# Optimization experiments

Hardware: AMD Instinct MI355X
Metric: run time of the kernel (lower is better)

Reference implementation:

```python
import jax, jax.numpy as jnp
import numpy as np

D_MODEL = 1024
NHEAD = 16
HEAD_DIM = D_MODEL // NHEAD


def setup_inputs() -> dict:
    key = jax.random.key(0)
    ks = jax.random.split(key, 11)
    B, S = 2, 2048
    s = 1.0 / np.sqrt(D_MODEL)
    return {
        "query": jax.random.normal(ks[0], (B, S, D_MODEL), jnp.float32),
        "key": jax.random.normal(ks[1], (B, S, D_MODEL), jnp.float32),
        "value": jax.random.normal(ks[2], (B, S, D_MODEL), jnp.float32),
        "wq_w": jax.random.normal(ks[3], (D_MODEL, D_MODEL), jnp.float32) * s,
        "wq_b": jax.random.normal(ks[4], (D_MODEL,), jnp.float32) * s,
        "wk_w": jax.random.normal(ks[5], (D_MODEL, D_MODEL), jnp.float32) * s,
        "wk_b": jax.random.normal(ks[6], (D_MODEL,), jnp.float32) * s,
        "wv_w": jax.random.normal(ks[7], (D_MODEL, D_MODEL), jnp.float32) * s,
        "wv_b": jax.random.normal(ks[8], (D_MODEL,), jnp.float32) * s,
        "wo_w": jax.random.normal(ks[9], (D_MODEL, D_MODEL), jnp.float32) * s,
        "wo_b": jax.random.normal(ks[10], (D_MODEL,), jnp.float32) * s,
    }


def reference(query, key, value, wq_w, wq_b, wk_w, wk_b, wv_w, wv_b, wo_w, wo_b):
    B, S, _ = query.shape
    # torch Linear: x @ W.T + b
    def proj(x, w, b):
        y = x @ w.T + b
        return y.reshape(B, S, NHEAD, HEAD_DIM).transpose(0, 2, 1, 3)  # [B,H,S,Dh]

    Q = proj(query, wq_w, wq_b)
    K = proj(key, wk_w, wk_b)
    V = proj(value, wv_w, wv_b)

    scale = 1.0 / np.sqrt(HEAD_DIM).astype(np.float32)
    scores = jnp.einsum("bhqd,bhkd->bhqk", Q, K) * scale  # [B,H,S,S]
    causal = jnp.tril(jnp.ones((S, S), dtype=bool))
    scores = jnp.where(causal, scores, -jnp.inf)
    attn = jax.nn.softmax(scores, axis=-1)
    out = jnp.einsum("bhqk,bhkd->bhqd", attn, V)  # [B,H,S,Dh]
    out = out.transpose(0, 2, 1, 3).reshape(B, S, D_MODEL)
    return out @ wo_w.T + wo_b
```

## Files before the change

kernel.cpp:

```cpp
#include <hip/hip_runtime.h>
#include <stdint.h>

#define D_MODEL 1024
#define S_LEN   2048
#define NHEAD   16
#define HEAD_DIM 64
#define BATCH   2
#define M_TOT   (BATCH * S_LEN)
#define Q_SCALE 0.18033688011112042f

using bf16x8 = __attribute__((ext_vector_type(8))) short;
using f32x4  = __attribute__((ext_vector_type(4))) float;

__device__ __forceinline__ unsigned short f2bf(float f) {
  union { float f; unsigned int u; } v; v.f = f;
  unsigned int u = v.u;
  return (unsigned short)((u + 0x7FFFu + ((u >> 16) & 1u)) >> 16);
}
__device__ __forceinline__ unsigned int pkbf(float a, float b) {
#if __has_builtin(__builtin_amdgcn_cvt_pk_bf16_f32)
  auto p = __builtin_amdgcn_cvt_pk_bf16_f32(a, b);
  union { decltype(p) v; unsigned int u; } c; c.v = p;
  return c.u;
#else
  return (unsigned int)f2bf(a) | ((unsigned int)f2bf(b) << 16);
#endif
}
__device__ __forceinline__ bf16x8 cvt8(const float* p) {
  const float4 a = *(const float4*)p;
  const float4 b = *(const float4*)(p + 4);
  union { unsigned int u[4]; bf16x8 v; } r;
  r.u[0] = pkbf(a.x, a.y); r.u[1] = pkbf(a.z, a.w);
  r.u[2] = pkbf(b.x, b.y); r.u[3] = pkbf(b.z, b.w);
  return r.v;
}
__device__ __forceinline__ float fexp2(float x) {
#if __has_builtin(__builtin_amdgcn_exp2f)
  return __builtin_amdgcn_exp2f(x);
#else
  return __expf(x * 0.69314718055994531f);
#endif
}
__device__ __forceinline__ void async16(const unsigned short* g, short* l) {
  __builtin_amdgcn_global_load_lds(
      reinterpret_cast<const __attribute__((address_space(1))) unsigned int*>(
          reinterpret_cast<uintptr_t>(g)),
      reinterpret_cast<__attribute__((address_space(3))) unsigned int*>(
          reinterpret_cast<uintptr_t>(l)),
      16, 0, 0);
}

__device__ __forceinline__ void swap32(unsigned int& x, unsigned int& y) {
#if __has_builtin(__builtin_amdgcn_permlane32_swap)
  auto r = __builtin_amdgcn_permlane32_swap(x, y, false, false);
  x = (unsigned int)r[0]; y = (unsigned int)r[1];
#else
  const int lane = threadIdx.x & 63;
  unsigned int sx = (unsigned int)__shfl_xor((int)x, 32);
  unsigned int sy = (unsigned int)__shfl_xor((int)y, 32);
  unsigned int nx = (lane & 32) ? sy : x;
  unsigned int ny = (lane & 32) ? y : sx;
  x = nx; y = ny;
#endif
}
__device__ __forceinline__ void swap16(unsigned int& x, unsigned int& y) {
#if __has_builtin(__builtin_amdgcn_permlane16_swap)
  auto r = __builtin_amdgcn_permlane16_swap(x, y, false, false);
  x = (unsigned int)r[0]; y = (unsigned int)r[1];
#else
  const int lane = threadIdx.x & 63;
  unsigned int sx = (unsigned int)__shfl_xor((int)x, 16);
  unsigned int sy = (unsigned int)__shfl_xor((int)y, 16);
  unsigned int nx = (lane & 16) ? sy : x;
  unsigned int ny = (lane & 16) ? y : sx;
  x = nx; y = ny;
#endif
}

#define LDK 40

__global__ __launch_bounds__(256)
void cast_all(const float* __restrict__ wq, const float* __restrict__ wk,
              const float* __restrict__ wv, const float* __restrict__ wo,
              const float* __restrict__ q, const float* __restrict__ k,
              const float* __restrict__ v,
              unsigned short* __restrict__ wb,
              unsigned short* __restrict__ qb, unsigned short* __restrict__ kb,
              unsigned short* __restrict__ vb)
{
  const int z = blockIdx.y;
  const float* src;
  unsigned short* d;
  size_t n;
  switch (z) {
    case 0: src = wq; d = wb;                                   n = (size_t)D_MODEL * D_MODEL; break;
    case 1: src = wk; d = wb + (size_t)1 * D_MODEL * D_MODEL;   n = (size_t)D_MODEL * D_MODEL; break;
    case 2: src = wv; d = wb + (size_t)2 * D_MODEL * D_MODEL;   n = (size_t)D_MODEL * D_MODEL; break;
    case 3: src = wo; d = wb + (size_t)3 * D_MODEL * D_MODEL;   n = (size_t)D_MODEL * D_MODEL; break;
    case 4: src = q;  d = qb;                                   n = (size_t)M_TOT * D_MODEL;   break;
    case 5: src = k;  d = kb;                                   n = (size_t)M_TOT * D_MODEL;   break;
    default: src = v; d = vb;                                   n = (size_t)M_TOT * D_MODEL;   break;
  }
  const size_t i = ((size_t)blockIdx.x * 256 + threadIdx.x) * 8;
  if (i < n) *(bf16x8*)(d + i) = cvt8(src + i);
}

__device__ __forceinline__ void gemm_tile_lds(const unsigned short* __restrict__ A,
                                              const unsigned short* __restrict__ W,
                                              int m0, int n0,
                                              short* As, short* Bs,
                                              f32x4 acc[4][4])
{
  const int t    = threadIdx.x;
  const int lane = t & 63;
  const int w    = t >> 6;
  const int quad = lane >> 4;
  const int l16  = lane & 15;
  const int wm   = (w >> 1) * 64;
  const int wn   = (w & 1) * 64;
  const int srow = w * 16 + (lane >> 2);
  const int scol = (lane & 3) * 8;

  for (int mt = 0; mt < 4; ++mt)
    for (int nt = 0; nt < 4; ++nt)
      acc[mt][nt] = f32x4{0.f, 0.f, 0.f, 0.f};

  for (int kt = 0; kt < D_MODEL / 32; ++kt) {
    const int kc = kt * 32 + scol;
    __syncthreads();
    async16(A + (size_t)(m0 + srow)      * D_MODEL + kc, As + srow * 32 + scol);
    async16(A + (size_t)(m0 + 64 + srow) * D_MODEL + kc, As + (64 + srow) * 32 + scol);
    async16(W + (size_t)(n0 + srow)      * D_MODEL + kc, Bs + srow * 32 + scol);
    async16(W + (size_t)(n0 + 64 + srow) * D_MODEL + kc, Bs + (64 + srow) * 32 + scol);
    __syncthreads();

    bf16x8 af[4], bfr[4];
    for (int mt = 0; mt < 4; ++mt)
      af[mt] = *(const bf16x8*)(As + (wm + mt * 16 + l16) * 32 + quad * 8);
    for (int nt = 0; nt < 4; ++nt)
      bfr[nt] = *(const bf16x8*)(Bs + (wn + nt * 16 + l16) * 32 + quad * 8);
    for (int mt = 0; mt < 4; ++mt)
      for (int nt = 0; nt < 4; ++nt)
        acc[mt][nt] = __builtin_amdgcn_mfma_f32_16x16x32_bf16(af[mt], bfr[nt], acc[mt][nt], 0, 0, 0);
  }
}

__device__ __forceinline__ void gemm_tile_f32(const float* __restrict__ A,
                                              const unsigned short* __restrict__ W,
                                              int m0, int n0,
                                              short* As, short* Bs,
                                              f32x4 acc[4][4])
{
  const int t    = threadIdx.x;
  const int lane = t & 63;
  const int w    = t >> 6;
  const int quad = lane >> 4;
  const int l16  = lane & 15;
  const int wm   = (w >> 1) * 64;
  const int wn   = (w & 1) * 64;
  const int srow = t >> 2;
  const int scol = (t & 3) * 8;

  for (int mt = 0; mt < 4; ++mt)
    for (int nt = 0; nt < 4; ++nt)
      acc[mt][nt] = f32x4{0.f, 0.f, 0.f, 0.f};

  for (int kt = 0; kt < D_MODEL / 32; ++kt) {
    const int kc = kt * 32 + scol;
    const bf16x8 a0 = cvt8(A + (size_t)(m0 + srow)      * D_MODEL + kc);
    const bf16x8 a1 = cvt8(A + (size_t)(m0 + srow + 64) * D_MODEL + kc);
    const bf16x8 b0 = *(const bf16x8*)(W + (size_t)(n0 + srow)      * D_MODEL + kc);
    const bf16x8 b1 = *(const bf16x8*)(W + (size_t)(n0 + srow + 64) * D_MODEL + kc);
    __syncthreads();
    *(bf16x8*)(As + (srow)      * LDK + scol) = a0;
    *(bf16x8*)(As + (srow + 64) * LDK + scol) = a1;
    *(bf16x8*)(Bs + (srow)      * LDK + scol) = b0;
    *(bf16x8*)(Bs + (srow + 64) * LDK + scol) = b1;
    __syncthreads();

    bf16x8 af[4], bfr[4];
    for (int mt = 0; mt < 4; ++mt)
      af[mt] = *(const bf16x8*)(As + (wm + mt * 16 + l16) * LDK + quad * 8);
    for (int nt = 0; nt < 4; ++nt)
      bfr[nt] = *(const bf16x8*)(Bs + (wn + nt * 16 + l16) * LDK + quad * 8);
    for (int mt = 0; mt < 4; ++mt)
      for (int nt = 0; nt < 4; ++nt)
        acc[mt][nt] = __builtin_amdgcn_mfma_f32_16x16x32_bf16(af[mt], bfr[nt], acc[mt][nt], 0, 0, 0);
  }
}

__device__ __forceinline__ void qkv_epilogue(int z, int m0, int n0,
                                             const float* __restrict__ bias,
                                             float scale,
                                             unsigned short* __restrict__ dst,
                                             f32x4 acc[4][4])
{
  const int t    = threadIdx.x;
  const int lane = t & 63;
  const int w    = t >> 6;
  const int quad = lane >> 4;
  const int l16  = lane & 15;
  const int wm   = (w >> 1) * 64;
  const int wn   = (w & 1) * 64;

  for (int nt = 0; nt < 4; ++nt) {
    const int n = n0 + wn + nt * 16 + l16;
    const float bb = bias[n];
    const int h = n >> 6, d = n & 63;
    for (int mt = 0; mt < 4; ++mt) {
      for (int r = 0; r < 4; ++r) {
        const int m = m0 + wm + mt * 16 + quad * 4 + r;
        const int b = m >> 11, s = m & 2047;
        const unsigned short val = f2bf((acc[mt][nt][r] + bb) * scale);
        if (z < 2)
          dst[((size_t)((b * NHEAD + h) * S_LEN + s)) * HEAD_DIM + d] = val;
        else
          dst[((size_t)((b * NHEAD + h) * HEAD_DIM + d)) * S_LEN + s] = val;
      }
    }
  }
}

__global__ __launch_bounds__(256)
void qkv_fast(const unsigned short* __restrict__ qb,
              const unsigned short* __restrict__ kb,
              const unsigned short* __restrict__ vb,
              const unsigned short* __restrict__ wqb,
              const unsigned short* __restrict__ wkb,
              const unsigned short* __restrict__ wvb,
              const float* __restrict__ bq, const float* __restrict__ bk,
              const float* __restrict__ bv,
              unsigned short* __restrict__ Qh, unsigned short* __restrict__ Kh,
              unsigned short* __restrict__ VhT)
{
  __shared__ __attribute__((aligned(16))) short As[128 * 32];
  __shared__ __attribute__((aligned(16))) short Bs[128 * 32];
  const int z = blockIdx.z;
  const unsigned short* A    = (z == 0) ? qb  : (z == 1) ? kb  : vb;
  const unsigned short* W    = (z == 0) ? wqb : (z == 1) ? wkb : wvb;
  const float*          bias = (z == 0) ? bq  : (z == 1) ? bk  : bv;
  unsigned short*       dst  = (z == 0) ? Qh  : (z == 1) ? Kh  : VhT;
  const float           scale = (z == 0) ? Q_SCALE : 1.0f;

  const int m0 = blockIdx.x * 128, n0 = blockIdx.y * 128;
  f32x4 acc[4][4];
  gemm_tile_lds(A, W, m0, n0, As, Bs, acc);
  qkv_epilogue(z, m0, n0, bias, scale, dst, acc);
}

__global__ __launch_bounds__(256)
void qkv_slow(const float* __restrict__ query, const float* __restrict__ key,
              const float* __restrict__ value,
              const unsigned short* __restrict__ wqb,
              const unsigned short* __restrict__ wkb,
              const unsigned short* __restrict__ wvb,
              const float* __restrict__ bq, const float* __restrict__ bk,
              const float* __restrict__ bv,
              unsigned short* __restrict__ Qh, unsigned short* __restrict__ Kh,
              unsigned short* __restrict__ VhT)
{
  __shared__ __attribute__((aligned(16))) short As[128 * LDK];
  __shared__ __attribute__((aligned(16))) short Bs[128 * LDK];
  const int z = blockIdx.z;
  const float*          A    = (z == 0) ? query : (z == 1) ? key : value;
  const unsigned short* W    = (z == 0) ? wqb   : (z == 1) ? wkb : wvb;
  const float*          bias = (z == 0) ? bq    : (z == 1) ? bk  : bv;
  unsigned short*       dst  = (z == 0) ? Qh    : (z == 1) ? Kh  : VhT;
  const float           scale = (z == 0) ? Q_SCALE : 1.0f;

  const int m0 = blockIdx.x * 128, n0 = blockIdx.y * 128;
  f32x4 acc[4][4];
  gemm_tile_f32(A, W, m0, n0, As, Bs, acc);
  qkv_epilogue(z, m0, n0, bias, scale, dst, acc);
}

__global__ __launch_bounds__(256)
void out_proj(const unsigned short* __restrict__ Oh,
              const unsigned short* __restrict__ wob,
              const float* __restrict__ bo,
              float* __restrict__ dst)
{
  __shared__ __attribute__((aligned(16))) short As[64 * 32];
  __shared__ __attribute__((aligned(16))) short Bs[128 * 32];
  const int m0 = blockIdx.x * 64, n0 = blockIdx.y * 128;

  const int t    = threadIdx.x;
  const int lane = t & 63;
  const int w    = t >> 6;
  const int quad = lane >> 4;
  const int l16  = lane & 15;
  const int wm   = (w >> 1) * 32;
  const int wn   = (w & 1) * 64;
  const int srow = t >> 2;
  const int scol = (t & 3) * 8;

  f32x4 acc[2][4];
  for (int mt = 0; mt < 2; ++mt)
    for (int nt = 0; nt < 4; ++nt)
      acc[mt][nt] = f32x4{0.f, 0.f, 0.f, 0.f};

  for (int kt = 0; kt < D_MODEL / 32; ++kt) {
    const int kc = kt * 32 + scol;
    __syncthreads();
    async16(Oh  + (size_t)(m0 + srow)      * D_MODEL + kc, As + srow * 32 + scol);
    async16(wob + (size_t)(n0 + srow)      * D_MODEL + kc, Bs + srow * 32 + scol);
    async16(wob + (size_t)(n0 + 64 + srow) * D_MODEL + kc, Bs + (64 + srow) * 32 + scol);
    __syncthreads();

    bf16x8 af[2], bfr[4];
    for (int mt = 0; mt < 2; ++mt)
      af[mt] = *(const bf16x8*)(As + (wm + mt * 16 + l16) * 32 + quad * 8);
    for (int nt = 0; nt < 4; ++nt)
      bfr[nt] = *(const bf16x8*)(Bs + (wn + nt * 16 + l16) * 32 + quad * 8);
    for (int mt = 0; mt < 2; ++mt)
      for (int nt = 0; nt < 4; ++nt)
        acc[mt][nt] = __builtin_amdgcn_mfma_f32_16x16x32_bf16(af[mt], bfr[nt], acc[mt][nt], 0, 0, 0);
  }

  for (int nt = 0; nt < 4; ++nt) {
    const int n = n0 + wn + nt * 16 + l16;
    const float bb = bo[n];
    for (int mt = 0; mt < 2; ++mt)
      for (int r = 0; r < 4; ++r) {
        const int m = m0 + wm + mt * 16 + quad * 4 + r;
        dst[(size_t)m * D_MODEL + n] = acc[mt][nt][r] + bb;
      }
  }
}

struct Frags { bf16x8 ka0, ka1, kb0, kb1, v0, v1, v2, v3; };
struct StageRegs { bf16x8 k0, k1, k2, k3, v0, v1, v2, v3; };

#define KS_LD 72
#define VT_LD 136

__device__ __forceinline__ StageRegs load_stage(const unsigned short* __restrict__ Kb,
                                                const unsigned short* __restrict__ Vb,
                                                int k0, int kr, int kc, int vd, int vc) {
  StageRegs r;
  r.k0 = *(const bf16x8*)(Kb + (size_t)(k0 + kr)      * HEAD_DIM + kc);
  r.k1 = *(const bf16x8*)(Kb + (size_t)(k0 + kr + 32) * HEAD_DIM + kc);
  r.k2 = *(const bf16x8*)(Kb + (size_t)(k0 + kr + 64) * HEAD_DIM + kc);
  r.k3 = *(const bf16x8*)(Kb + (size_t)(k0 + kr + 96) * HEAD_DIM + kc);
  r.v0 = *(const bf16x8*)(Vb + (size_t)(vd)      * S_LEN + k0 + vc);
  r.v1 = *(const bf16x8*)(Vb + (size_t)(vd + 16) * S_LEN + k0 + vc);
  r.v2 = *(const bf16x8*)(Vb + (size_t)(vd + 32) * S_LEN + k0 + vc);
  r.v3 = *(const bf16x8*)(Vb + (size_t)(vd + 48) * S_LEN + k0 + vc);
  return r;
}
__device__ __forceinline__ void write_stage(const StageRegs& r, short* Ks, short* Vts,
                                            int kr, int kc, int vd, int vc) {
  *(bf16x8*)(Ks + (kr)      * KS_LD + kc) = r.k0;
  *(bf16x8*)(Ks + (kr + 32) * KS_LD + kc) = r.k1;
  *(bf16x8*)(Ks + (kr + 64) * KS_LD + kc) = r.k2;
  *(bf16x8*)(Ks + (kr + 96) * KS_LD + kc) = r.k3;
  *(bf16x8*)(Vts + (vd)      * VT_LD + vc) = r.v0;
  *(bf16x8*)(Vts + (vd + 16) * VT_LD + vc) = r.v1;
  *(bf16x8*)(Vts + (vd + 32) * VT_LD + vc) = r.v2;
  *(bf16x8*)(Vts + (vd + 48) * VT_LD + vc) = r.v3;
}
__device__ __forceinline__ Frags lds_frags(const short* Ks, const short* Vts,
                                           int c, int quad, int l16) {
  Frags f;
  const short* kp = Ks + (c * 32 + l16) * KS_LD + quad * 8;
  f.ka0 = *(const bf16x8*)(kp);
  f.ka1 = *(const bf16x8*)(kp + 32);
  f.kb0 = *(const bf16x8*)(kp + 16 * KS_LD);
  f.kb1 = *(const bf16x8*)(kp + 16 * KS_LD + 32);
  const short* vp = Vts + l16 * VT_LD + c * 32 + quad * 8;
  f.v0 = *(const bf16x8*)(vp);
  f.v1 = *(const bf16x8*)(vp + 16 * VT_LD);
  f.v2 = *(const bf16x8*)(vp + 32 * VT_LD);
  f.v3 = *(const bf16x8*)(vp + 48 * VT_LD);
  return f;
}

template <bool DIAG>
__device__ __forceinline__ void proc_chunk(const Frags& f, const bf16x8 qf[2][2],
                                           const bf16x8& ones, int quad, int l16,
                                           f32x4 lacc[2], f32x4 oacc[2][4]) {
  f32x4 sA0 = f32x4{0.f, 0.f, 0.f, 0.f};
  f32x4 sA1 = f32x4{0.f, 0.f, 0.f, 0.f};
  f32x4 sB0 = f32x4{0.f, 0.f, 0.f, 0.f};
  f32x4 sB1 = f32x4{0.f, 0.f, 0.f, 0.f};
  __builtin_amdgcn_s_setprio(1);
  sA0 = __builtin_amdgcn_mfma_f32_16x16x32_bf16(f.ka0, qf[0][0], sA0, 0, 0, 0);
  sA0 = __builtin_amdgcn_mfma_f32_16x16x32_bf16(f.ka1, qf[0][1], sA0, 0, 0, 0);
  sA1 = __builtin_amdgcn_mfma_f32_16x16x32_bf16(f.ka0, qf[1][0], sA1, 0, 0, 0);
  sA1 = __builtin_amdgcn_mfma_f32_16x16x32_bf16(f.ka1, qf[1][1], sA1, 0, 0, 0);
  if (!DIAG) {
    sB0 = __builtin_amdgcn_mfma_f32_16x16x32_bf16(f.kb0, qf[0][0], sB0, 0, 0, 0);
    sB0 = __builtin_amdgcn_mfma_f32_16x16x32_bf16(f.kb1, qf[0][1], sB0, 0, 0, 0);
  }
  sB1 = __builtin_amdgcn_mfma_f32_16x16x32_bf16(f.kb0, qf[1][0], sB1, 0, 0, 0);
  sB1 = __builtin_amdgcn_mfma_f32_16x16x32_bf16(f.kb1, qf[1][1], sB1, 0, 0, 0);
  __builtin_amdgcn_s_setprio(0);

  float stA0[4], stB0[4], stA1[4], stB1[4];
  const int kl = quad * 4;
#pragma unroll
  for (int r = 0; r < 4; ++r) {
    if (!DIAG) {
      stA0[r] = fexp2(sA0[r]);
      stB0[r] = fexp2(sB0[r]);
      stB1[r] = fexp2(sB1[r]);
    } else {
      stA0[r] = (kl + r <= l16) ? fexp2(sA0[r]) : 0.f;
      stB0[r] = 0.f;
      stB1[r] = (kl + r <= l16) ? fexp2(sB1[r]) : 0.f;
    }
    stA1[r] = fexp2(sA1[r]);
  }

  unsigned int a0 = pkbf(stA0[0], stA0[1]), b0 = pkbf(stA0[2], stA0[3]);
  unsigned int c0_ = pkbf(stB0[0], stB0[1]), e0 = pkbf(stB0[2], stB0[3]);
  swap32(a0, c0_); swap32(b0, e0);
  swap16(a0, c0_); swap16(b0, e0);
  union { unsigned int u[4]; bf16x8 v; } p0;
  p0.u[0] = a0; p0.u[1] = b0; p0.u[2] = c0_; p0.u[3] = e0;
  unsigned int a1 = pkbf(stA1[0], stA1[1]), b1 = pkbf(stA1[2], stA1[3]);
  unsigned int c1_ = pkbf(stB1[0], stB1[1]), e1 = pkbf(stB1[2], stB1[3]);
  swap32(a1, c1_); swap32(b1, e1);
  swap16(a1, c1_); swap16(b1, e1);
  union { unsigned int u[4]; bf16x8 v; } p1;
  p1.u[0] = a1; p1.u[1] = b1; p1.u[2] = c1_; p1.u[3] = e1;

  __builtin_amdgcn_s_setprio(1);
  lacc[0] = __builtin_amdgcn_mfma_f32_16x16x32_bf16(p0.v, ones, lacc[0], 0, 0, 0);
  lacc[1] = __builtin_amdgcn_mfma_f32_16x16x32_bf16(p1.v, ones, lacc[1], 0, 0, 0);
  oacc[0][0] = __builtin_amdgcn_mfma_f32_16x16x32_bf16(p0.v, f.v0, oacc[0][0], 0, 0, 0);
  oacc[1][0] = __builtin_amdgcn_mfma_f32_16x16x32_bf16(p1.v, f.v0, oacc[1][0], 0, 0, 0);
  oacc[0][1] = __builtin_amdgcn_mfma_f32_16x16x32_bf16(p0.v, f.v1, oacc[0][1], 0, 0, 0);
  oacc[1][1] = __builtin_amdgcn_mfma_f32_16x16x32_bf16(p1.v, f.v1, oacc[1][1], 0, 0, 0);
  oacc[0][2] = __builtin_amdgcn_mfma_f32_16x16x32_bf16(p0.v, f.v2, oacc[0][2], 0, 0, 0);
  oacc[1][2] = __builtin_amdgcn_mfma_f32_16x16x32_bf16(p1.v, f.v2, oacc[1][2], 0, 0, 0);
  oacc[0][3] = __builtin_amdgcn_mfma_f32_16x16x32_bf16(p0.v, f.v3, oacc[0][3], 0, 0, 0);
  oacc[1][3] = __builtin_amdgcn_mfma_f32_16x16x32_bf16(p1.v, f.v3, oacc[1][3], 0, 0, 0);
  __builtin_amdgcn_s_setprio(0);
}

__global__ __launch_bounds__(256)
void attn_kernel(const unsigned short* __restrict__ Qh,
                 const unsigned short* __restrict__ Kh,
                 const unsigned short* __restrict__ VhT,
                 unsigned short* __restrict__ O)
{
  __shared__ __attribute__((aligned(16))) short Ks[2][128 * KS_LD];
  __shared__ __attribute__((aligned(16))) short Vts[2][64 * VT_LD];

  const int orig = blockIdx.x;
  const int xcd  = orig & 7;
  const int li   = orig >> 3;
  const int bh   = xcd * 4 + (li & 3);
  const int qt   = 15 - (li >> 2);
  const int q0   = qt * 128;
  const int b    = bh >> 4;
  const int h    = bh & 15;
  const int t    = threadIdx.x;
  const int w    = t >> 6;
  const int lane = t & 63;
  const int quad = lane >> 4;
  const int l16  = lane & 15;
  const int rowbase = q0 + w * 32;

  const unsigned short* Kb = Kh + (size_t)bh * S_LEN * HEAD_DIM;
  const unsigned short* Vb = VhT + (size_t)bh * HEAD_DIM * S_LEN;
  const int kr = t >> 3, kc = (t & 7) * 8;
  const int vd = t >> 4, vc = (t & 15) * 8;

  bf16x8 qf[2][2];
#pragma unroll
  for (int mt = 0; mt < 2; ++mt) {
    const size_t qrow = (size_t)bh * S_LEN + rowbase + mt * 16 + l16;
    qf[mt][0] = *(const bf16x8*)(Qh + qrow * HEAD_DIM + quad * 8);
    qf[mt][1] = *(const bf16x8*)(Qh + qrow * HEAD_DIM + 32 + quad * 8);
  }
  bf16x8 ones;
#pragma unroll
  for (int j = 0; j < 8; ++j) ones[j] = (short)0x3F80;

  f32x4 lacc[2];
  f32x4 oacc[2][4];
  lacc[0] = f32x4{0.f, 0.f, 0.f, 0.f};
  lacc[1] = f32x4{0.f, 0.f, 0.f, 0.f};
#pragma unroll
  for (int mt = 0; mt < 2; ++mt)
#pragma unroll
    for (int dt = 0; dt < 4; ++dt) oacc[mt][dt] = f32x4{0.f, 0.f, 0.f, 0.f};

  const int nT = qt + 1;
  StageRegs rs = load_stage(Kb, Vb, 0, kr, kc, vd, vc);
  write_stage(rs, Ks[0], Vts[0], kr, kc, vd, vc);
  __syncthreads();
  for (int j = 0; j < nT; ++j) {
    const short* Ksj = (j & 1) ? Ks[1] : Ks[0];
    const short* Vtj = (j & 1) ? Vts[1] : Vts[0];
    short* Ksn = (j & 1) ? Ks[0] : Ks[1];
    short* Vtn = (j & 1) ? Vts[0] : Vts[1];
    const bool more = (j + 1 < nT);
    if (more) rs = load_stage(Kb, Vb, (j + 1) * 128, kr, kc, vd, vc);
    if (j < qt) {
#pragma unroll
      for (int c = 0; c < 4; ++c) {
        const Frags f = lds_frags(Ksj, Vtj, c, quad, l16);
        proc_chunk<false>(f, qf, ones, quad, l16, lacc, oacc);
      }
    } else {
      for (int c = 0; c < w; ++c) {
        const Frags f = lds_frags(Ksj, Vtj, c, quad, l16);
        proc_chunk<false>(f, qf, ones, quad, l16, lacc, oacc);
      }
      const Frags f = lds_frags(Ksj, Vtj, w, quad, l16);
      proc_chunk<true>(f, qf, ones, quad, l16, lacc, oacc);
    }
    if (more) write_stage(rs, Ksn, Vtn, kr, kc, vd, vc);
    __syncthreads();
  }

#pragma unroll
  for (int mt = 0; mt < 2; ++mt)
#pragma unroll
    for (int dt = 0; dt < 4; ++dt)
#pragma unroll
      for (int r = 0; r < 4; ++r) {
        const int rowg = rowbase + mt * 16 + quad * 4 + r;
        O[(size_t)(b * S_LEN + rowg) * D_MODEL + h * 64 + dt * 16 + l16] =
            f2bf(oacc[mt][dt][r] / lacc[mt][r]);
      }
}

extern "C" void kernel_launch(void* const* d_in, const int* in_sizes, int n_in,
                              void* d_out, int out_size, void* d_ws, size_t ws_size,
                              hipStream_t stream)
{
  (void)in_sizes; (void)n_in; (void)out_size;
  const float* q  = (const float*)d_in[0];
  const float* k  = (const float*)d_in[1];
  const float* v  = (const float*)d_in[2];
  const float* wq = (const float*)d_in[3];
  const float* bq = (const float*)d_in[4];
  const float* wk = (const float*)d_in[5];
  const float* bk = (const float*)d_in[6];
  const float* wv = (const float*)d_in[7];
  const float* bv = (const float*)d_in[8];
  const float* wo = (const float*)d_in[9];
  const float* bo = (const float*)d_in[10];
  float* out = (float*)d_out;

  unsigned short* wb  = (unsigned short*)d_ws;
  unsigned short* wqb = wb;
  unsigned short* wkb = wb + (size_t)1 * D_MODEL * D_MODEL;
  unsigned short* wvb = wb + (size_t)2 * D_MODEL * D_MODEL;
  unsigned short* wob = wb + (size_t)3 * D_MODEL * D_MODEL;
  unsigned short* Kh  = wb + (size_t)4 * D_MODEL * D_MODEL;
  unsigned short* VhT = Kh + (size_t)M_TOT * D_MODEL;
  unsigned short* Oh  = VhT + (size_t)M_TOT * D_MODEL;
  unsigned short* qb  = Oh;
  unsigned short* vb  = Oh + (size_t)M_TOT * D_MODEL;
  unsigned short* Qh  = (unsigned short*)d_out;
  unsigned short* kb  = Qh + (size_t)M_TOT * D_MODEL;

  const bool fast = ws_size >= (size_t)40 * 1024 * 1024;

  dim3 g1(M_TOT / 128, D_MODEL / 128, 3);
  if (fast) {
    dim3 gc((size_t)M_TOT * D_MODEL / (256 * 8), 7, 1);
    cast_all<<<gc, 256, 0, stream>>>(wq, wk, wv, wo, q, k, v, wb, qb, kb, vb);
    qkv_fast<<<g1, 256, 0, stream>>>(qb, kb, vb, wqb, wkb, wvb, bq, bk, bv, Qh, Kh, VhT);
  } else {
    dim3 gc((size_t)D_MODEL * D_MODEL / (256 * 8), 4, 1);
    cast_all<<<gc, 256, 0, stream>>>(wq, wk, wv, wo, q, k, v, wb, qb, kb, vb);
    qkv_slow<<<g1, 256, 0, stream>>>(q, k, v, wqb, wkb, wvb, bq, bk, bv, Qh, Kh, VhT);
  }

  dim3 g2(512, 1, 1);
  attn_kernel<<<g2, 256, 0, stream>>>(Qh, Kh, VhT, Oh);

  dim3 g3(M_TOT / 64, D_MODEL / 128, 1);
  out_proj<<<g3, 256, 0, stream>>>(Oh, wob, bo, out);
}
```

Measured before the change: 216.6 us.

## Split attention work across 8 waves with 16 query rows each

The attention kernel now launches 512 threads per block instead of 256, and each wave owns 16 query rows instead of 32. The K/V staging loads are spread over twice as many threads, so each thread stages half as much. The diagonal-tile masking is rewritten into three modes to handle the finer split. The intent is more waves per CU and fewer registers per thread, to hide latency better. The cost is less reuse of each K/V fragment read from LDS per MFMA, giving more LDS traffic per unit of work.

```diff
diff --git a/kernel.cpp b/kernel.cpp
--- a/kernel.cpp
+++ b/kernel.cpp
@@ -329,7 +329,7 @@
 }
 
 struct Frags { bf16x8 ka0, ka1, kb0, kb1, v0, v1, v2, v3; };
-struct StageRegs { bf16x8 k0, k1, k2, k3, v0, v1, v2, v3; };
+struct StageRegs { bf16x8 k0, k1, v0, v1; };
 
 #define KS_LD 72
 #define VT_LD 136
@@ -339,25 +339,17 @@
                                                 int k0, int kr, int kc, int vd, int vc) {
   StageRegs r;
   r.k0 = *(const bf16x8*)(Kb + (size_t)(k0 + kr)      * HEAD_DIM + kc);
-  r.k1 = *(const bf16x8*)(Kb + (size_t)(k0 + kr + 32) * HEAD_DIM + kc);
-  r.k2 = *(const bf16x8*)(Kb + (size_t)(k0 + kr + 64) * HEAD_DIM + kc);
-  r.k3 = *(const bf16x8*)(Kb + (size_t)(k0 + kr + 96) * HEAD_DIM + kc);
+  r.k1 = *(const bf16x8*)(Kb + (size_t)(k0 + kr + 64) * HEAD_DIM + kc);
   r.v0 = *(const bf16x8*)(Vb + (size_t)(vd)      * S_LEN + k0 + vc);
-  r.v1 = *(const bf16x8*)(Vb + (size_t)(vd + 16) * S_LEN + k0 + vc);
-  r.v2 = *(const bf16x8*)(Vb + (size_t)(vd + 32) * S_LEN + k0 + vc);
-  r.v3 = *(const bf16x8*)(Vb + (size_t)(vd + 48) * S_LEN + k0 + vc);
+  r.v1 = *(const bf16x8*)(Vb + (size_t)(vd + 32) * S_LEN + k0 + vc);
   return r;
 }
 __device__ __forceinline__ void write_stage(const StageRegs& r, short* Ks, short* Vts,
                                             int kr, int kc, int vd, int vc) {
   *(bf16x8*)(Ks + (kr)      * KS_LD + kc) = r.k0;
-  *(bf16x8*)(Ks + (kr + 32) * KS_LD + kc) = r.k1;
-  *(bf16x8*)(Ks + (kr + 64) * KS_LD + kc) = r.k2;
-  *(bf16x8*)(Ks + (kr + 96) * KS_LD + kc) = r.k3;
+  *(bf16x8*)(Ks + (kr + 64) * KS_LD + kc) = r.k1;
   *(bf16x8*)(Vts + (vd)      * VT_LD + vc) = r.v0;
-  *(bf16x8*)(Vts + (vd + 16) * VT_LD + vc) = r.v1;
-  *(bf16x8*)(Vts + (vd + 32) * VT_LD + vc) = r.v2;
-  *(bf16x8*)(Vts + (vd + 48) * VT_LD + vc) = r.v3;
+  *(bf16x8*)(Vts + (vd + 32) * VT_LD + vc) = r.v1;
 }
 __device__ __forceinline__ Frags lds_frags(const short* Ks, const short* Vts,
                                            int c, int quad, int l16) {
@@ -375,71 +367,54 @@
   return f;
 }
 
-template <bool DIAG>
-__device__ __forceinline__ void proc_chunk(const Frags& f, const bf16x8 qf[2][2],
+template <int MODE>
+__device__ __forceinline__ void proc_chunk(const Frags& f, const bf16x8 qf[2],
                                            const bf16x8& ones, int quad, int l16,
-                                           f32x4 lacc[2], f32x4 oacc[2][4]) {
-  f32x4 sA0 = f32x4{0.f, 0.f, 0.f, 0.f};
-  f32x4 sA1 = f32x4{0.f, 0.f, 0.f, 0.f};
-  f32x4 sB0 = f32x4{0.f, 0.f, 0.f, 0.f};
-  f32x4 sB1 = f32x4{0.f, 0.f, 0.f, 0.f};
+                                           f32x4& lacc, f32x4 oacc[4]) {
+  f32x4 s0 = f32x4{0.f, 0.f, 0.f, 0.f};
+  f32x4 s1 = f32x4{0.f, 0.f, 0.f, 0.f};
   __builtin_amdgcn_s_setprio(1);
-  sA0 = __builtin_amdgcn_mfma_f32_16x16x32_bf16(f.ka0, qf[0][0], sA0, 0, 0, 0);
-  sA0 = __builtin_amdgcn_mfma_f32_16x16x32_bf16(f.ka1, qf[0][1], sA0, 0, 0, 0);
-  sA1 = __builtin_amdgcn_mfma_f32_16x16x32_bf16(f.ka0, qf[1][0], sA1, 0, 0, 0);
-  sA1 = __builtin_amdgcn_mfma_f32_16x16x32_bf16(f.ka1, qf[1][1], sA1, 0, 0, 0);
-  if (!DIAG) {
-    sB0 = __builtin_amdgcn_mfma_f32_16x16x32_bf16(f.kb0, qf[0][0], sB0, 0, 0, 0);
-    sB0 = __builtin_amdgcn_mfma_f32_16x16x32_bf16(f.kb1, qf[0][1], sB0, 0, 0, 0);
-  }
-  sB1 = __builtin_amdgcn_mfma_f32_16x16x32_bf16(f.kb0, qf[1][0], sB1, 0, 0, 0);
-  sB1 = __builtin_amdgcn_mfma_f32_16x16x32_bf16(f.kb1, qf[1][1], sB1, 0, 0, 0);
+  s0 = __builtin_amdgcn_mfma_f32_16x16x32_bf16(f.ka0, qf[0], s0, 0, 0, 0);
+  s0 = __builtin_amdgcn_mfma_f32_16x16x32_bf16(f.ka1, qf[1], s0, 0, 0, 0);
+  if (MODE != 1) {
+    s1 = __builtin_amdgcn_mfma_f32_16x16x32_bf16(f.kb0, qf[0], s1, 0, 0, 0);
+    s1 = __builtin_amdgcn_mfma_f32_16x16x32_bf16(f.kb1, qf[1], s1, 0, 0, 0);
+  }
   __builtin_amdgcn_s_setprio(0);
 
-  float stA0[4], stB0[4], stA1[4], stB1[4];
+  float st0[4], st1[4];
   const int kl = quad * 4;
 #pragma unroll
   for (int r = 0; r < 4; ++r) {
-    if (!DIAG) {
-      stA0[r] = fexp2(sA0[r]);
-      stB0[r] = fexp2(sB0[r]);
-      stB1[r] = fexp2(sB1[r]);
+    if (MODE == 0) {
+      st0[r] = fexp2(s0[r]);
+      st1[r] = fexp2(s1[r]);
+    } else if (MODE == 1) {
+      st0[r] = (kl + r <= l16) ? fexp2(s0[r]) : 0.f;
+      st1[r] = 0.f;
     } else {
-      stA0[r] = (kl + r <= l16) ? fexp2(sA0[r]) : 0.f;
-      stB0[r] = 0.f;
-      stB1[r] = (kl + r <= l16) ? fexp2(sB1[r]) : 0.f;
+      st0[r] = fexp2(s0[r]);
+      st1[r] = (kl + r <= l16) ? fexp2(s1[r]) : 0.f;
     }
-    stA1[r] = fexp2(sA1[r]);
-  }
-
-  unsigned int a0 = pkbf(stA0[0], stA0[1]), b0 = pkbf(stA0[2], stA0[3]);
-  unsigned int c0_ = pkbf(stB0[0], stB0[1]), e0 = pkbf(stB0[2], stB0[3]);
-  swap32(a0, c0_); swap32(b0, e0);
-  swap16(a0, c0_); swap16(b0, e0);
-  union { unsigned int u[4]; bf16x8 v; } p0;
-  p0.u[0] = a0; p0.u[1] = b0; p0.u[2] = c0_; p0.u[3] = e0;
-  unsigned int a1 = pkbf(stA1[0], stA1[1]), b1 = pkbf(stA1[2], stA1[3]);
-  unsigned int c1_ = pkbf(stB1[0], stB1[1]), e1 = pkbf(stB1[2], stB1[3]);
-  swap32(a1, c1_); swap32(b1, e1);
-  swap16(a1, c1_); swap16(b1, e1);
-  union { unsigned int u[4]; bf16x8 v; } p1;
-  p1.u[0] = a1; p1.u[1] = b1; p1.u[2] = c1_; p1.u[3] = e1;
+  }
+
+  unsigned int a = pkbf(st0[0], st0[1]), b = pkbf(st0[2], st0[3]);
+  unsigned int c = pkbf(st1[0], st1[1]), e = pkbf(st1[2], st1[3]);
+  swap32(a, c); swap32(b, e);
+  swap16(a, c); swap16(b, e);
+  union { unsigned int u[4]; bf16x8 v; } pf;
+  pf.u[0] = a; pf.u[1] = b; pf.u[2] = c; pf.u[3] = e;
 
   __builtin_amdgcn_s_setprio(1);
-  lacc[0] = __builtin_amdgcn_mfma_f32_16x16x32_bf16(p0.v, ones, lacc[0], 0, 0, 0);
-  lacc[1] = __builtin_amdgcn_mfma_f32_16x16x32_bf16(p1.v, ones, lacc[1], 0, 0, 0);
-  oacc[0][0] = __builtin_amdgcn_mfma_f32_16x16x32_bf16(p0.v, f.v0, oacc[0][0], 0, 0, 0);
-  oacc[1][0] = __builtin_amdgcn_mfma_f32_16x16x32_bf16(p1.v, f.v0, oacc[1][0], 0, 0, 0);
-  oacc[0][1] = __builtin_amdgcn_mfma_f32_16x16x32_bf16(p0.v, f.v1, oacc[0][1], 0, 0, 0);
-  oacc[1][1] = __builtin_amdgcn_mfma_f32_16x16x32_bf16(p1.v, f.v1, oacc[1][1], 0, 0, 0);
-  oacc[0][2] = __builtin_amdgcn_mfma_f32_16x16x32_bf16(p0.v, f.v2, oacc[0][2], 0, 0, 0);
-  oacc[1][2] = __builtin_amdgcn_mfma_f32_16x16x32_bf16(p1.v, f.v2, oacc[1][2], 0, 0, 0);
-  oacc[0][3] = __builtin_amdgcn_mfma_f32_16x16x32_bf16(p0.v, f.v3, oacc[0][3], 0, 0, 0);
-  oacc[1][3] = __builtin_amdgcn_mfma_f32_16x16x32_bf16(p1.v, f.v3, oacc[1][3], 0, 0, 0);
+  lacc = __builtin_amdgcn_mfma_f32_16x16x32_bf16(pf.v, ones, lacc, 0, 0, 0);
+  oacc[0] = __builtin_amdgcn_mfma_f32_16x16x32_bf16(pf.v, f.v0, oacc[0], 0, 0, 0);
+  oacc[1] = __builtin_amdgcn_mfma_f32_16x16x32_bf16(pf.v, f.v1, oacc[1], 0, 0, 0);
+  oacc[2] = __builtin_amdgcn_mfma_f32_16x16x32_bf16(pf.v, f.v2, oacc[2], 0, 0, 0);
+  oacc[3] = __builtin_amdgcn_mfma_f32_16x16x32_bf16(pf.v, f.v3, oacc[3], 0, 0, 0);
   __builtin_amdgcn_s_setprio(0);
 }
 
-__global__ __launch_bounds__(256)
+__global__ __launch_bounds__(512, 4)
 void attn_kernel(const unsigned short* __restrict__ Qh,
                  const unsigned short* __restrict__ Kh,
                  const unsigned short* __restrict__ VhT,
@@ -461,34 +436,32 @@
   const int lane = t & 63;
   const int quad = lane >> 4;
   const int l16  = lane & 15;
-  const int rowbase = q0 + w * 32;
+  const int rowbase = q0 + w * 16;
 
   const unsigned short* Kb = Kh + (size_t)bh * S_LEN * HEAD_DIM;
   const unsigned short* Vb = VhT + (size_t)bh * HEAD_DIM * S_LEN;
   const int kr = t >> 3, kc = (t & 7) * 8;
   const int vd = t >> 4, vc = (t & 15) * 8;
 
-  bf16x8 qf[2][2];
-#pragma unroll
-  for (int mt = 0; mt < 2; ++mt) {
-    const size_t qrow = (size_t)bh * S_LEN + rowbase + mt * 16 + l16;
-    qf[mt][0] = *(const bf16x8*)(Qh + qrow * HEAD_DIM + quad * 8);
-    qf[mt][1] = *(const bf16x8*)(Qh + qrow * HEAD_DIM + 32 + quad * 8);
+  bf16x8 qf[2];
+  {
+    const size_t qrow = (size_t)bh * S_LEN + rowbase + l16;
+    qf[0] = *(const bf16x8*)(Qh + qrow * HEAD_DIM + quad * 8);
+    qf[1] = *(const bf16x8*)(Qh + qrow * HEAD_DIM + 32 + quad * 8);
   }
   bf16x8 ones;
 #pragma unroll
   for (int j = 0; j < 8; ++j) ones[j] = (short)0x3F80;
 
-  f32x4 lacc[2];
-  f32x4 oacc[2][4];
-  lacc[0] = f32x4{0.f, 0.f, 0.f, 0.f};
-  lacc[1] = f32x4{0.f, 0.f, 0.f, 0.f};
+  f32x4 lacc = f32x4{0.f, 0.f, 0.f, 0.f};
+  f32x4 oacc[4];
 #pragma unroll
-  for (int mt = 0; mt < 2; ++mt)
-#pragma unroll
-    for (int dt = 0; dt < 4; ++dt) oacc[mt][dt] = f32x4{0.f, 0.f, 0.f, 0.f};
+  for (int dt = 0; dt < 4; ++dt) oacc[dt] = f32x4{0.f, 0.f, 0.f, 0.f};
 
   const int nT = qt + 1;
+  const int cw = w >> 1;
+  const bool odd = (w & 1) != 0;
+
   StageRegs rs = load_stage(Kb, Vb, 0, kr, kc, vd, vc);
   write_stage(rs, Ks[0], Vts[0], kr, kc, vd, vc);
   __syncthreads();
@@ -503,30 +476,29 @@
 #pragma unroll
       for (int c = 0; c < 4; ++c) {
         const Frags f = lds_frags(Ksj, Vtj, c, quad, l16);
-        proc_chunk<false>(f, qf, ones, quad, l16, lacc, oacc);
+        proc_chunk<0>(f, qf, ones, quad, l16, lacc, oacc);
       }
     } else {
-      for (int c = 0; c < w; ++c) {
+      for (int c = 0; c < cw; ++c) {
         const Frags f = lds_frags(Ksj, Vtj, c, quad, l16);
-        proc_chunk<false>(f, qf, ones, quad, l16, lacc, oacc);
+        proc_chunk<0>(f, qf, ones, quad, l16, lacc, oacc);
       }
-      const Frags f = lds_frags(Ksj, Vtj, w, quad, l16);
-      proc_chunk<true>(f, qf, ones, quad, l16, lacc, oacc);
+      const Frags f = lds_frags(Ksj, Vtj, cw, quad, l16);
+      if (odd) proc_chunk<2>(f, qf, ones, quad, l16, lacc, oacc);
+      else     proc_chunk<1>(f, qf, ones, quad, l16, lacc, oacc);
     }
     if (more) write_stage(rs, Ksn, Vtn, kr, kc, vd, vc);
     __syncthreads();
   }
 
 #pragma unroll
-  for (int mt = 0; mt < 2; ++mt)
+  for (int dt = 0; dt < 4; ++dt)
 #pragma unroll
-    for (int dt = 0; dt < 4; ++dt)
-#pragma unroll
-      for (int r = 0; r < 4; ++r) {
-        const int rowg = rowbase + mt * 16 + quad * 4 + r;
-        O[(size_t)(b * S_LEN + rowg) * D_MODEL + h * 64 + dt * 16 + l16] =
-            f2bf(oacc[mt][dt][r] / lacc[mt][r]);
-      }
+    for (int r = 0; r < 4; ++r) {
+      const int rowg = rowbase + quad * 4 + r;
+      O[(size_t)(b * S_LEN + rowg) * D_MODEL + h * 64 + dt * 16 + l16] =
+          f2bf(oacc[dt][r] / lacc[r]);
+    }
 }
 
 extern "C" void kernel_launch(void* const* d_in, const int* in_sizes, int n_in,
@@ -574,7 +546,7 @@
   }
 
   dim3 g2(512, 1, 1);
-  attn_kernel<<<g2, 256, 0, stream>>>(Qh, Kh, VhT, Oh);
+  attn_kernel<<<g2, 512, 0, stream>>>(Qh, Kh, VhT, Oh);
 
   dim3 g3(M_TOT / 64, D_MODEL / 128, 1);
   out_proj<<<g3, 256, 0, stream>>>(Oh, wob, bo, out);
```

Measured after the change: 214.2 us. Within noise of the previous version (-1.1%).
